# Performance work log

Hardware: AMD Instinct MI355X
Metric: run time of the kernel (lower is better)

The kernel has to match this reference:

```python
import jax, jax.numpy as jnp
import numpy as np

N_NODES = 50000
N_EDGES = 800000
D_IN = 128
HIDDEN = 128
N_GRAPHS = 64


def gcn_conv(x, src, dst, W, b, num_nodes):
    """PyG GCNConv: out = D^{-1/2} (A+I) D^{-1/2} (x W) + b.
    src/dst already include self-loops."""
    h = x @ W  # [N, out]
    deg = jax.ops.segment_sum(jnp.ones_like(dst, dtype=h.dtype), dst,
                              num_segments=num_nodes)  # in-degree incl. self loop
    dinv = jnp.where(deg > 0, jax.lax.rsqrt(jnp.maximum(deg, 1e-12)), 0.0)
    norm = dinv[src] * dinv[dst]  # [E+N]
    msgs = h[src] * norm[:, None]  # gather + scale
    out = jax.ops.segment_sum(msgs, dst, num_segments=num_nodes)
    return out + b


def setup_inputs() -> dict:
    key = jax.random.key(0)
    ks = jax.random.split(key, 8)
    x = jax.random.normal(ks[0], (N_NODES, D_IN), dtype=jnp.float32)
    edge_index = jax.random.randint(ks[1], (2, N_EDGES), 0, N_NODES, dtype=jnp.int64)
    batch = jnp.sort(jax.random.randint(ks[2], (N_NODES,), 0, N_GRAPHS, dtype=jnp.int64))
    # Glorot-ish scaled params
    s = lambda fan_in: 1.0 / np.sqrt(fan_in)
    W1 = jax.random.normal(ks[3], (D_IN, HIDDEN), dtype=jnp.float32) * s(D_IN)
    b1 = jnp.zeros((HIDDEN,), dtype=jnp.float32)
    W2 = jax.random.normal(ks[4], (HIDDEN, HIDDEN), dtype=jnp.float32) * s(HIDDEN)
    b2 = jnp.zeros((HIDDEN,), dtype=jnp.float32)
    Wh1 = jax.random.normal(ks[5], (HIDDEN, HIDDEN), dtype=jnp.float32) * s(HIDDEN)
    bh1 = jnp.zeros((HIDDEN,), dtype=jnp.float32)
    Wh2 = jax.random.normal(ks[6], (HIDDEN, 1), dtype=jnp.float32) * s(HIDDEN)
    bh2 = jnp.zeros((1,), dtype=jnp.float32)
    return {"x": x, "edge_index": edge_index, "batch": batch,
            "W1": W1, "b1": b1, "W2": W2, "b2": b2,
            "Wh1": Wh1, "bh1": bh1, "Wh2": Wh2, "bh2": bh2}


def reference(x, edge_index, batch, W1, b1, W2, b2, Wh1, bh1, Wh2, bh2):
    n = x.shape[0]
    loop = jnp.arange(n, dtype=edge_index.dtype)
    src = jnp.concatenate([edge_index[0], loop])  # add self-loops once
    dst = jnp.concatenate([edge_index[1], loop])
    h = jax.nn.relu(gcn_conv(x, src, dst, W1, b1, n))
    h = jax.nn.relu(gcn_conv(h, src, dst, W2, b2, n))
    # global mean pool over graphs
    sums = jax.ops.segment_sum(h, batch, num_segments=N_GRAPHS)
    cnts = jax.ops.segment_sum(jnp.ones((n,), dtype=h.dtype), batch,
                               num_segments=N_GRAPHS)
    pooled = sums / jnp.maximum(cnts, 1.0)[:, None]  # [G, HIDDEN]
    # MLP head: Linear -> ReLU -> Linear -> Sigmoid -> squeeze(-1)
    z = jax.nn.relu(pooled @ Wh1 + bh1)
    out = jax.nn.sigmoid(z @ Wh2 + bh2)
    return out[:, 0]  # [G]
```

## Files before the change

### kernel.cpp

```cpp
#include <hip/hip_runtime.h>


#define NB 256
#define NBK 256

typedef __attribute__((ext_vector_type(8))) short bf16x8;
typedef __attribute__((ext_vector_type(4))) float f32x4;
typedef __attribute__((ext_vector_type(2))) float f32x2;

__device__ inline unsigned short f2bf(float f) {
    union { float f; unsigned int u; } c; c.f = f;
    unsigned int u = c.u + (0x7fffu + ((c.u >> 16) & 1u));
    return (unsigned short)(u >> 16);
}
__device__ inline float bf2f(unsigned short b) {
    union { unsigned int u; float f; } c; c.u = ((unsigned int)b) << 16;
    return c.f;
}

__device__ inline unsigned char f2fp8_sw(float f) {
    union { float f; unsigned int u; } c; c.f = f;
    unsigned int s = (c.u >> 24) & 0x80u;
    unsigned int au = c.u & 0x7FFFFFFFu;
    if (au >= 0x3C800000u) {
        if (au > 0x43E00000u) au = 0x43E00000u;
        unsigned int r = au + 0x000FFFFFu + ((au >> 20) & 1u);
        unsigned int e8 = (r >> 23) - 120u;
        unsigned int m8 = (r >> 20) & 7u;
        return (unsigned char)(s | (e8 << 3) | m8);
    }
    float av = c.f < 0.f ? -c.f : c.f;
    unsigned int M = (unsigned int)(av * 512.0f + 0.5f);
    return (unsigned char)(s | M);
}
__device__ inline float fp82f_sw(unsigned int cbyte) {
    unsigned int E = (cbyte >> 3) & 0xFu, M = cbyte & 7u;
    union { unsigned int u; float f; } v;
    v.u = ((E + 120u) << 23) | (M << 20);
    float r = E ? v.f : (float)M * 0.001953125f;
    return (cbyte & 0x80u) ? -r : r;
}

template <bool HI>
__device__ inline f32x2 fp8x2_f32(unsigned int u) {
#if __has_builtin(__builtin_amdgcn_cvt_pk_f32_fp8)
    return __builtin_amdgcn_cvt_pk_f32_fp8(u, HI);
#else
    unsigned int w = HI ? (u >> 16) : u;
    f32x2 r; r[0] = fp82f_sw(w & 0xFFu); r[1] = fp82f_sw((w >> 8) & 0xFFu);
    return r;
#endif
}
__device__ inline unsigned char f2fp8(float f) {
#if __has_builtin(__builtin_amdgcn_cvt_pk_fp8_f32)
    return (unsigned char)(__builtin_amdgcn_cvt_pk_fp8_f32(f, f, 0, false) & 0xFFu);
#else
    return f2fp8_sw(f);
#endif
}

__global__ __launch_bounds__(256) void k_hist(const int* __restrict__ dst,
                                              int* __restrict__ hist,
                                              float* __restrict__ sums,
                                              float* __restrict__ cnt,
                                              int ne, int chunk) {
    __shared__ int h[NBK];
    int t = threadIdx.x, b = blockIdx.x;
    h[t] = 0;
    int gid = b * 256 + t;
    if (gid < 64 * 128) sums[gid] = 0.0f;
    if (gid < 64) cnt[gid] = 0.0f;
    __syncthreads();
    int e0 = b * chunk, e1 = min(e0 + chunk, ne);
    for (int e = e0 + t; e < e1; e += 256) atomicAdd(&h[dst[e] >> 8], 1);
    __syncthreads();
    hist[b * NBK + t] = h[t];
}

__global__ __launch_bounds__(256) void k_scanb(int* __restrict__ hist,
                                               int* __restrict__ bstart,
                                               int* __restrict__ row_start,
                                               int n, int ne) {
    __shared__ int ps[256];
    int j = threadIdx.x;
    int run = 0;
    for (int i = 0; i < NB; ++i) {
        int t = hist[i * NBK + j];
        hist[i * NBK + j] = run;
        run += t;
    }
    ps[j] = run;
    __syncthreads();
    for (int off = 1; off < 256; off <<= 1) {
        int v = (j >= off) ? ps[j - off] : 0;
        __syncthreads();
        ps[j] += v;
        __syncthreads();
    }
    int excl = ps[j] - run;
    bstart[j] = excl;
    if (j == 255) bstart[256] = ps[255];
    if (j == 0) row_start[n] = ne;
    for (int i = 0; i < NB; ++i) hist[i * NBK + j] += excl;
}

__global__ __launch_bounds__(256) void k_scat(const int* __restrict__ src,
                                              const int* __restrict__ dst,
                                              const int* __restrict__ hist,
                                              unsigned int* __restrict__ ebuf,
                                              int ne, int chunk) {
    __shared__ int cur[NBK];
    int t = threadIdx.x, b = blockIdx.x;
    cur[t] = hist[b * NBK + t];
    __syncthreads();
    int e0 = b * chunk, e1 = min(e0 + chunk, ne);
    for (int e = e0 + t; e < e1; e += 256) {
        int d = dst[e];
        int p = atomicAdd(&cur[d >> 8], 1);
        ebuf[p] = ((unsigned int)(d & 255) << 24) | (unsigned int)src[e];
    }
}

__global__ __launch_bounds__(256) void k_bsort(const unsigned int* __restrict__ ebuf,
                                               const int* __restrict__ bstart,
                                               int* __restrict__ csr,
                                               int* __restrict__ row_start,
                                               float* __restrict__ dinv,
                                               int n) {
    __shared__ int h[NBK];
    __shared__ int sc[NBK];
    int j = threadIdx.x, b = blockIdx.x;
    int s0 = bstart[b], s1 = bstart[b + 1];
    h[j] = 0;
    __syncthreads();
    for (int e = s0 + j; e < s1; e += 256) atomicAdd(&h[ebuf[e] >> 24], 1);
    __syncthreads();
    sc[j] = h[j];
    __syncthreads();
    for (int off = 1; off < 256; off <<= 1) {
        int v = (j >= off) ? sc[j - off] : 0;
        __syncthreads();
        sc[j] += v;
        __syncthreads();
    }
    int excl = sc[j] - h[j];
    int id = b * 256 + j;
    int deg = h[j];
    if (id < n) {
        row_start[id] = s0 + excl;
        dinv[id] = rsqrtf((float)deg + 1.0f);
    }
    __syncthreads();
    h[j] = excl;
    __syncthreads();
    for (int e = s0 + j; e < s1; e += 256) {
        unsigned int pk = ebuf[e];
        int p = atomicAdd(&h[pk >> 24], 1);
        csr[s0 + p] = (int)(pk & 0x00FFFFFFu);
    }
}

__global__ __launch_bounds__(256) void k_castw(const float* __restrict__ W1,
                                               const float* __restrict__ W2,
                                               unsigned short* __restrict__ Wt1,
                                               unsigned short* __restrict__ Wt2) {
    int tid = blockIdx.x * 256 + threadIdx.x;
    int i = tid & 16383;
    int nn = i >> 7, kk = i & 127;
    if (tid < 16384) Wt1[i] = f2bf(W1[kk * 128 + nn]);
    else             Wt2[i] = f2bf(W2[kk * 128 + nn]);
}

template <bool F32IN>
__global__ __launch_bounds__(256) void k_gemm_mfma(const void* __restrict__ Xin,
                                                   const short* __restrict__ Wt,
                                                   unsigned char* __restrict__ Y8,
                                                   int n_rows) {
    int wid = threadIdx.x >> 6;
    int lane = threadIdx.x & 63;
    int r = lane & 15, q = lane >> 4;
    int m0 = blockIdx.x * 64;
    int n0 = wid * 32;
    unsigned char* Yp = Y8 + (size_t)(n0 >> 6) * n_rows * 64;
    int c0 = n0 & 63;

    bf16x8 bfr[2][4];
#pragma unroll
    for (int nt = 0; nt < 2; ++nt)
#pragma unroll
        for (int ks = 0; ks < 4; ++ks)
            bfr[nt][ks] = *(const bf16x8*)(Wt + (size_t)(n0 + nt * 16 + r) * 128 +
                                           ks * 32 + q * 8);

#pragma unroll
    for (int rt = 0; rt < 4; ++rt) {
        int row = m0 + rt * 16 + r;
        int rl = min(row, n_rows - 1);
        f32x4 acc0 = {0.f, 0.f, 0.f, 0.f};
        f32x4 acc1 = {0.f, 0.f, 0.f, 0.f};
#pragma unroll
        for (int ks = 0; ks < 4; ++ks) {
            bf16x8 a;
            if constexpr (F32IN) {
                const float* xr = (const float*)Xin + (size_t)rl * 128 + ks * 32 + q * 8;
                float4 f0 = *(const float4*)xr;
                float4 f1 = *(const float4*)(xr + 4);
                a[0] = (short)f2bf(f0.x); a[1] = (short)f2bf(f0.y);
                a[2] = (short)f2bf(f0.z); a[3] = (short)f2bf(f0.w);
                a[4] = (short)f2bf(f1.x); a[5] = (short)f2bf(f1.y);
                a[6] = (short)f2bf(f1.z); a[7] = (short)f2bf(f1.w);
            } else {
                a = *(const bf16x8*)((const short*)Xin + (size_t)rl * 128 + ks * 32 + q * 8);
            }
            acc0 = __builtin_amdgcn_mfma_f32_16x16x32_bf16(a, bfr[0][ks], acc0, 0, 0, 0);
            acc1 = __builtin_amdgcn_mfma_f32_16x16x32_bf16(a, bfr[1][ks], acc1, 0, 0, 0);
        }
#pragma unroll
        for (int v = 0; v < 4; ++v) {
            int orow = m0 + rt * 16 + q * 4 + v;
            if (orow < n_rows) {
                Yp[(size_t)orow * 64 + c0 + r]      = f2fp8(acc0[v]);
                Yp[(size_t)orow * 64 + c0 + 16 + r] = f2fp8(acc1[v]);
            }
        }
    }
}

__global__ __launch_bounds__(256) void k_aggp(const unsigned char* __restrict__ plane,
                                              const float* __restrict__ dinv,
                                              const int* __restrict__ csr,
                                              const int* __restrict__ row_start,
                                              const float* __restrict__ bias_ph,
                                              unsigned short* __restrict__ out,
                                              int n, int phofs) {
    int node = blockIdx.x * 4 + (threadIdx.x >> 6);
    if (node >= n) return;
    int lane = threadIdx.x & 63;
    int slot = lane >> 4, fi = lane & 15;
    const unsigned int* hp = (const unsigned int*)plane;

    float di = dinv[node];
    float selfw = (slot == 0) ? di * di : 0.0f;
    unsigned int hu = hp[(size_t)node * 16 + fi];
    f32x2 p0 = fp8x2_f32<false>(hu);
    f32x2 p1 = fp8x2_f32<true>(hu);
    float a0 = p0[0] * selfw, a1 = p0[1] * selfw;
    float a2 = p1[0] * selfw, a3 = p1[1] * selfw;

    int beg = row_start[node];
    int end = row_start[node + 1];
    int deg = end - beg;

    int mysrc = (lane < deg) ? csr[beg + lane] : 0;
    float myw = ((lane < deg) ? dinv[mysrc] : 0.0f) * di;

    int m = min(deg, 64);
    int e = 0;
    for (; e + 8 <= m; e += 8) {
        int i0 = e + slot, i1 = e + 4 + slot;
        int s0 = __shfl(mysrc, i0);
        int s1 = __shfl(mysrc, i1);
        float w0 = __shfl(myw, i0);
        float w1 = __shfl(myw, i1);
        unsigned int u0 = hp[(size_t)s0 * 16 + fi];
        unsigned int u1 = hp[(size_t)s1 * 16 + fi];
        f32x2 v00 = fp8x2_f32<false>(u0), v01 = fp8x2_f32<true>(u0);
        f32x2 v10 = fp8x2_f32<false>(u1), v11 = fp8x2_f32<true>(u1);
        a0 += v00[0] * w0; a1 += v00[1] * w0; a2 += v01[0] * w0; a3 += v01[1] * w0;
        a0 += v10[0] * w1; a1 += v10[1] * w1; a2 += v11[0] * w1; a3 += v11[1] * w1;
    }
    for (; e < m; e += 4) {
        int idx = e + slot;
        int s = __shfl(mysrc, idx & 63);
        float w = __shfl(myw, idx & 63);
        if (idx >= m) { s = 0; w = 0.0f; }
        unsigned int u = hp[(size_t)s * 16 + fi];
        f32x2 v0 = fp8x2_f32<false>(u), v1 = fp8x2_f32<true>(u);
        a0 += v0[0] * w; a1 += v0[1] * w; a2 += v1[0] * w; a3 += v1[1] * w;
    }
    if (slot == 0) {
        for (int j = beg + 64; j < end; ++j) {
            int s = csr[j];
            float w = dinv[s] * di;
            unsigned int u = hp[(size_t)s * 16 + fi];
            f32x2 v0 = fp8x2_f32<false>(u), v1 = fp8x2_f32<true>(u);
            a0 += v0[0] * w; a1 += v0[1] * w; a2 += v1[0] * w; a3 += v1[1] * w;
        }
    }

    a0 += __shfl_xor(a0, 16); a0 += __shfl_xor(a0, 32);
    a1 += __shfl_xor(a1, 16); a1 += __shfl_xor(a1, 32);
    a2 += __shfl_xor(a2, 16); a2 += __shfl_xor(a2, 32);
    a3 += __shfl_xor(a3, 16); a3 += __shfl_xor(a3, 32);

    if (slot == 0) {
        float4 bv = ((const float4*)bias_ph)[fi];
        float o0 = fmaxf(a0 + bv.x, 0.0f);
        float o1 = fmaxf(a1 + bv.y, 0.0f);
        float o2 = fmaxf(a2 + bv.z, 0.0f);
        float o3 = fmaxf(a3 + bv.w, 0.0f);
        uint2 pk;
        pk.x = (unsigned int)f2bf(o0) | ((unsigned int)f2bf(o1) << 16);
        pk.y = (unsigned int)f2bf(o2) | ((unsigned int)f2bf(o3) << 16);
        *(uint2*)(out + (size_t)node * 128 + phofs + fi * 4) = pk;
    }
}

#define POOL_CHUNK 64
__global__ __launch_bounds__(128) void k_pool(const unsigned short* __restrict__ h,
                                              const int* __restrict__ batch,
                                              float* __restrict__ sums,
                                              float* __restrict__ cnt, int n) {
    int d = threadIdx.x;
    int c0 = blockIdx.x * POOL_CHUNK;
    if (c0 >= n) return;
    int c1 = min(c0 + POOL_CHUNK, n);
    float acc = 0.f, cc = 0.f;
    int g_cur = batch[c0];
    for (int i = c0; i < c1; ++i) {
        int g = batch[i];
        if (g != g_cur) {
            atomicAdd(&sums[g_cur * 128 + d], acc);
            if (d == 0) atomicAdd(&cnt[g_cur], cc);
            acc = 0.f; cc = 0.f; g_cur = g;
        }
        acc += bf2f(h[(size_t)i * 128 + d]);
        cc += 1.f;
    }
    atomicAdd(&sums[g_cur * 128 + d], acc);
    if (d == 0) atomicAdd(&cnt[g_cur], cc);
}

__global__ __launch_bounds__(128) void k_head(const float* __restrict__ sums,
                                              const float* __restrict__ cnt,
                                              const float* __restrict__ Wh1,
                                              const float* __restrict__ bh1,
                                              const float* __restrict__ Wh2,
                                              const float* __restrict__ bh2,
                                              float* __restrict__ out) {
    int g = blockIdx.x;
    int d = threadIdx.x;
    __shared__ float sp[128];
    __shared__ float red[128];
    float c = fmaxf(cnt[g], 1.0f);
    sp[d] = sums[g * 128 + d] / c;
    __syncthreads();
    float acc = bh1[d];
    for (int k = 0; k < 128; ++k) acc += sp[k] * Wh1[k * 128 + d];
    float z = fmaxf(acc, 0.f);
    red[d] = z * Wh2[d];
    __syncthreads();
    for (int off = 64; off > 0; off >>= 1) {
        if (d < off) red[d] += red[d + off];
        __syncthreads();
    }
    if (d == 0) out[g] = 1.f / (1.f + expf(-(red[0] + bh2[0])));
}

extern "C" void kernel_launch(void* const* d_in, const int* in_sizes, int n_in,
                              void* d_out, int out_size, void* d_ws,
                              size_t ws_size, hipStream_t stream) {
    const float* x    = (const float*)d_in[0];
    const int*   ei   = (const int*)d_in[1];
    const int*   batch= (const int*)d_in[2];
    const float* W1   = (const float*)d_in[3];
    const float* b1   = (const float*)d_in[4];
    const float* W2   = (const float*)d_in[5];
    const float* b2   = (const float*)d_in[6];
    const float* Wh1  = (const float*)d_in[7];
    const float* bh1  = (const float*)d_in[8];
    const float* Wh2  = (const float*)d_in[9];
    const float* bh2  = (const float*)d_in[10];
    float* out = (float*)d_out;

    const int n  = in_sizes[0] / 128;
    const int ne = in_sizes[1] / 2;
    const int* src = ei;
    const int* dst = ei + ne;

    char* p = (char*)d_ws;
    int* hist      = (int*)p;  p += (size_t)NB * NBK * 4;
    int* bstart    = (int*)p;  p += 257 * 4;
    int* row_start = (int*)p;  p += (size_t)(n + 1) * 4;
    float* dinv    = (float*)p; p += (size_t)n * 4;
    unsigned int* ebuf = (unsigned int*)p; p += (size_t)ne * 4;
    int* csr       = (int*)p;  p += (size_t)ne * 4;
    p = (char*)(((uintptr_t)p + 15) & ~(uintptr_t)15);
    unsigned short* Wt1 = (unsigned short*)p; p += 128 * 128 * 2;
    unsigned short* Wt2 = (unsigned short*)p; p += 128 * 128 * 2;
    unsigned char* h8   = (unsigned char*)p; p += (size_t)n * 128;
    p = (char*)(((uintptr_t)p + 15) & ~(uintptr_t)15);
    unsigned short* abf = (unsigned short*)p; p += (size_t)n * 128 * 2;
    p = (char*)(((uintptr_t)p + 15) & ~(uintptr_t)15);
    float* sums = (float*)p;   p += (size_t)64 * 128 * 4;
    float* cnt  = (float*)p;

    int chunk = (ne + NB - 1) / NB;
    int nb_g = (n + 63) / 64;
    int nb_a = (n + 3) / 4;
    int nb_p = (n + POOL_CHUNK - 1) / POOL_CHUNK;
    size_t plane = (size_t)n * 64;

    k_hist<<<NB, 256, 0, stream>>>(dst, hist, sums, cnt, ne, chunk);
    k_scanb<<<1, 256, 0, stream>>>(hist, bstart, row_start, n, ne);
    k_scat<<<NB, 256, 0, stream>>>(src, dst, hist, ebuf, ne, chunk);
    k_bsort<<<256, 256, 0, stream>>>(ebuf, bstart, csr, row_start, dinv, n);

    k_castw<<<128, 256, 0, stream>>>(W1, W2, Wt1, Wt2);

    k_gemm_mfma<true><<<nb_g, 256, 0, stream>>>((const void*)x, (const short*)Wt1, h8, n);
    k_aggp<<<nb_a, 256, 0, stream>>>(h8,         dinv, csr, row_start, b1,      abf, n, 0);
    k_aggp<<<nb_a, 256, 0, stream>>>(h8 + plane, dinv, csr, row_start, b1 + 64, abf, n, 64);

    k_gemm_mfma<false><<<nb_g, 256, 0, stream>>>((const void*)abf, (const short*)Wt2, h8, n);
    k_aggp<<<nb_a, 256, 0, stream>>>(h8,         dinv, csr, row_start, b2,      abf, n, 0);
    k_aggp<<<nb_a, 256, 0, stream>>>(h8 + plane, dinv, csr, row_start, b2 + 64, abf, n, 64);

    k_pool<<<nb_p, 128, 0, stream>>>(abf, batch, sums, cnt, n);
    k_head<<<64, 128, 0, stream>>>(sums, cnt, Wh1, bh1, Wh2, bh2, out);
}
```

Baseline: 212.7 us.

## Replace split-plane fp8 layout with row-major layout and single aggregation pass

The GEMM now writes fp8 features row-major (128 bytes per node) instead of two 64-column planes. Each layer then uses one aggregation kernel instead of two: 32 lanes cover all 128 features and the wave processes two edges at a time. This removes a second pass over the CSR, dinv and index shuffles, and drops one launch per layer. In exchange each gathered row is 128 bytes instead of 64, and a plane no longer fits in cache on its own, so the gather working set doubles.

```diff
diff --git a/kernel.cpp b/kernel.cpp
--- a/kernel.cpp
+++ b/kernel.cpp
@@ -181,8 +181,6 @@
     int r = lane & 15, q = lane >> 4;
     int m0 = blockIdx.x * 64;
     int n0 = wid * 32;
-    unsigned char* Yp = Y8 + (size_t)(n0 >> 6) * n_rows * 64;
-    int c0 = n0 & 63;
 
     bf16x8 bfr[2][4];
 #pragma unroll
@@ -219,29 +217,29 @@
         for (int v = 0; v < 4; ++v) {
             int orow = m0 + rt * 16 + q * 4 + v;
             if (orow < n_rows) {
-                Yp[(size_t)orow * 64 + c0 + r]      = f2fp8(acc0[v]);
-                Yp[(size_t)orow * 64 + c0 + 16 + r] = f2fp8(acc1[v]);
+                Y8[(size_t)orow * 128 + n0 + r]      = f2fp8(acc0[v]);
+                Y8[(size_t)orow * 128 + n0 + 16 + r] = f2fp8(acc1[v]);
             }
         }
     }
 }
 
-__global__ __launch_bounds__(256) void k_aggp(const unsigned char* __restrict__ plane,
-                                              const float* __restrict__ dinv,
-                                              const int* __restrict__ csr,
-                                              const int* __restrict__ row_start,
-                                              const float* __restrict__ bias_ph,
-                                              unsigned short* __restrict__ out,
-                                              int n, int phofs) {
+__global__ __launch_bounds__(256) void k_agg(const unsigned char* __restrict__ h8,
+                                             const float* __restrict__ dinv,
+                                             const int* __restrict__ csr,
+                                             const int* __restrict__ row_start,
+                                             const float* __restrict__ bias,
+                                             unsigned short* __restrict__ out,
+                                             int n) {
     int node = blockIdx.x * 4 + (threadIdx.x >> 6);
     if (node >= n) return;
     int lane = threadIdx.x & 63;
-    int slot = lane >> 4, fi = lane & 15;
-    const unsigned int* hp = (const unsigned int*)plane;
+    int s = lane >> 5, fi = lane & 31;
+    const unsigned int* hp = (const unsigned int*)h8;
 
     float di = dinv[node];
-    float selfw = (slot == 0) ? di * di : 0.0f;
-    unsigned int hu = hp[(size_t)node * 16 + fi];
+    float selfw = (s == 0) ? di * di : 0.0f;
+    unsigned int hu = hp[(size_t)node * 32 + fi];
     f32x2 p0 = fp8x2_f32<false>(hu);
     f32x2 p1 = fp8x2_f32<true>(hu);
     float a0 = p0[0] * selfw, a1 = p0[1] * selfw;
@@ -257,44 +255,57 @@
     int m = min(deg, 64);
     int e = 0;
     for (; e + 8 <= m; e += 8) {
-        int i0 = e + slot, i1 = e + 4 + slot;
+        int i0 = e + s, i1 = e + 2 + s, i2 = e + 4 + s, i3 = e + 6 + s;
         int s0 = __shfl(mysrc, i0);
         int s1 = __shfl(mysrc, i1);
+        int s2 = __shfl(mysrc, i2);
+        int s3 = __shfl(mysrc, i3);
         float w0 = __shfl(myw, i0);
         float w1 = __shfl(myw, i1);
-        unsigned int u0 = hp[(size_t)s0 * 16 + fi];
-        unsigned int u1 = hp[(size_t)s1 * 16 + fi];
-        f32x2 v00 = fp8x2_f32<false>(u0), v01 = fp8x2_f32<true>(u0);
-        f32x2 v10 = fp8x2_f32<false>(u1), v11 = fp8x2_f32<true>(u1);
-        a0 += v00[0] * w0; a1 += v00[1] * w0; a2 += v01[0] * w0; a3 += v01[1] * w0;
-        a0 += v10[0] * w1; a1 += v10[1] * w1; a2 += v11[0] * w1; a3 += v11[1] * w1;
-    }
-    for (; e < m; e += 4) {
-        int idx = e + slot;
-        int s = __shfl(mysrc, idx & 63);
+        float w2 = __shfl(myw, i2);
+        float w3 = __shfl(myw, i3);
+        unsigned int u0 = hp[(size_t)s0 * 32 + fi];
+        unsigned int u1 = hp[(size_t)s1 * 32 + fi];
+        unsigned int u2 = hp[(size_t)s2 * 32 + fi];
+        unsigned int u3 = hp[(size_t)s3 * 32 + fi];
+        f32x2 v;
+        v = fp8x2_f32<false>(u0); a0 += v[0] * w0; a1 += v[1] * w0;
+        v = fp8x2_f32<true>(u0);  a2 += v[0] * w0; a3 += v[1] * w0;
+        v = fp8x2_f32<false>(u1); a0 += v[0] * w1; a1 += v[1] * w1;
+        v = fp8x2_f32<true>(u1);  a2 += v[0] * w1; a3 += v[1] * w1;
+        v = fp8x2_f32<false>(u2); a0 += v[0] * w2; a1 += v[1] * w2;
+        v = fp8x2_f32<true>(u2);  a2 += v[0] * w2; a3 += v[1] * w2;
+        v = fp8x2_f32<false>(u3); a0 += v[0] * w3; a1 += v[1] * w3;
+        v = fp8x2_f32<true>(u3);  a2 += v[0] * w3; a3 += v[1] * w3;
+    }
+    for (; e < m; e += 2) {
+        int idx = e + s;
+        int sx = __shfl(mysrc, idx & 63);
         float w = __shfl(myw, idx & 63);
-        if (idx >= m) { s = 0; w = 0.0f; }
-        unsigned int u = hp[(size_t)s * 16 + fi];
-        f32x2 v0 = fp8x2_f32<false>(u), v1 = fp8x2_f32<true>(u);
-        a0 += v0[0] * w; a1 += v0[1] * w; a2 += v1[0] * w; a3 += v1[1] * w;
-    }
-    if (slot == 0) {
+        if (idx >= m) w = 0.0f;
+        unsigned int u = hp[(size_t)sx * 32 + fi];
+        f32x2 v;
+        v = fp8x2_f32<false>(u); a0 += v[0] * w; a1 += v[1] * w;
+        v = fp8x2_f32<true>(u);  a2 += v[0] * w; a3 += v[1] * w;
+    }
+    if (s == 0) {
         for (int j = beg + 64; j < end; ++j) {
-            int s = csr[j];
-            float w = dinv[s] * di;
-            unsigned int u = hp[(size_t)s * 16 + fi];
-            f32x2 v0 = fp8x2_f32<false>(u), v1 = fp8x2_f32<true>(u);
-            a0 += v0[0] * w; a1 += v0[1] * w; a2 += v1[0] * w; a3 += v1[1] * w;
+            int sx = csr[j];
+            float w = dinv[sx] * di;
+            unsigned int u = hp[(size_t)sx * 32 + fi];
+            f32x2 v;
+            v = fp8x2_f32<false>(u); a0 += v[0] * w; a1 += v[1] * w;
+            v = fp8x2_f32<true>(u);  a2 += v[0] * w; a3 += v[1] * w;
         }
     }
 
-    a0 += __shfl_xor(a0, 16); a0 += __shfl_xor(a0, 32);
-    a1 += __shfl_xor(a1, 16); a1 += __shfl_xor(a1, 32);
-    a2 += __shfl_xor(a2, 16); a2 += __shfl_xor(a2, 32);
-    a3 += __shfl_xor(a3, 16); a3 += __shfl_xor(a3, 32);
-
-    if (slot == 0) {
-        float4 bv = ((const float4*)bias_ph)[fi];
+    a0 += __shfl_xor(a0, 32);
+    a1 += __shfl_xor(a1, 32);
+    a2 += __shfl_xor(a2, 32);
+    a3 += __shfl_xor(a3, 32);
+
+    if (s == 0) {
+        float4 bv = ((const float4*)bias)[fi];
         float o0 = fmaxf(a0 + bv.x, 0.0f);
         float o1 = fmaxf(a1 + bv.y, 0.0f);
         float o2 = fmaxf(a2 + bv.z, 0.0f);
@@ -302,7 +313,7 @@
         uint2 pk;
         pk.x = (unsigned int)f2bf(o0) | ((unsigned int)f2bf(o1) << 16);
         pk.y = (unsigned int)f2bf(o2) | ((unsigned int)f2bf(o3) << 16);
-        *(uint2*)(out + (size_t)node * 128 + phofs + fi * 4) = pk;
+        *(uint2*)(out + (size_t)node * 128 + fi * 4) = pk;
     }
 }
 
@@ -399,7 +410,6 @@
     int nb_g = (n + 63) / 64;
     int nb_a = (n + 3) / 4;
     int nb_p = (n + POOL_CHUNK - 1) / POOL_CHUNK;
-    size_t plane = (size_t)n * 64;
 
     k_hist<<<NB, 256, 0, stream>>>(dst, hist, sums, cnt, ne, chunk);
     k_scanb<<<1, 256, 0, stream>>>(hist, bstart, row_start, n, ne);
@@ -409,12 +419,10 @@
     k_castw<<<128, 256, 0, stream>>>(W1, W2, Wt1, Wt2);
 
     k_gemm_mfma<true><<<nb_g, 256, 0, stream>>>((const void*)x, (const short*)Wt1, h8, n);
-    k_aggp<<<nb_a, 256, 0, stream>>>(h8,         dinv, csr, row_start, b1,      abf, n, 0);
-    k_aggp<<<nb_a, 256, 0, stream>>>(h8 + plane, dinv, csr, row_start, b1 + 64, abf, n, 64);
+    k_agg<<<nb_a, 256, 0, stream>>>(h8, dinv, csr, row_start, b1, abf, n);
 
     k_gemm_mfma<false><<<nb_g, 256, 0, stream>>>((const void*)abf, (const short*)Wt2, h8, n);
-    k_aggp<<<nb_a, 256, 0, stream>>>(h8,         dinv, csr, row_start, b2,      abf, n, 0);
-    k_aggp<<<nb_a, 256, 0, stream>>>(h8 + plane, dinv, csr, row_start, b2 + 64, abf, n, 64);
+    k_agg<<<nb_a, 256, 0, stream>>>(h8, dinv, csr, row_start, b2, abf, n);
 
     k_pool<<<nb_p, 128, 0, stream>>>(abf, batch, sums, cnt, n);
     k_head<<<64, 128, 0, stream>>>(sums, cnt, Wh1, bh1, Wh2, bh2, out);
```

Result: faster. 182.4 us (-14.3%).
